# Kernel tuning notes

Measured on AMD Instinct MI355X. Metric: run time of the kernel, lower is better.

Reference implementation:

```python
import jax, jax.numpy as jnp
import numpy as np

B, S, D, H, DFF = 2, 2048, 1024, 16, 4096
DK = D // H
EPS = 1e-6
MASK_FILL = -1.0  # original code uses -1**9 == -1 (precedence bug), NOT -1e9


def layernorm(x, gamma, beta):
    # original: (x - mean) / (std + eps), std unbiased (torch default ddof=1), scalar gamma/beta
    mean = jnp.mean(x, axis=-1, keepdims=True)
    std = jnp.std(x, axis=-1, keepdims=True, ddof=1)
    return gamma * (x - mean) / (std + EPS) + beta


def setup_inputs() -> dict:
    key = jax.random.key(0)
    ks = jax.random.split(key, 12)
    sc = 0.02
    return {
        "x": jax.random.normal(ks[0], (B, S, D), jnp.float32),
        "src_mask": jnp.ones((B, 1, 1, S), jnp.int32),
        "wq": jax.random.normal(ks[1], (D, D), jnp.float32) * sc,
        "bq": jnp.zeros((D,), jnp.float32),
        "wk": jax.random.normal(ks[2], (D, D), jnp.float32) * sc,
        "bk": jnp.zeros((D,), jnp.float32),
        "wv": jax.random.normal(ks[3], (D, D), jnp.float32) * sc,
        "bv": jnp.zeros((D,), jnp.float32),
        "wo": jax.random.normal(ks[4], (D, D), jnp.float32) * sc,
        "bo": jnp.zeros((D,), jnp.float32),
        "w1": jax.random.normal(ks[5], (D, DFF), jnp.float32) * sc,
        "b1": jnp.zeros((DFF,), jnp.float32),
        "w2": jax.random.normal(ks[6], (DFF, D), jnp.float32) * sc,
        "b2": jnp.zeros((D,), jnp.float32),
        "g1": jnp.ones((), jnp.float32),
        "be1": jnp.zeros((), jnp.float32),
        "g2": jnp.ones((), jnp.float32),
        "be2": jnp.zeros((), jnp.float32),
    }


def reference(x, src_mask, wq, bq, wk, bk, wv, bv, wo, bo,
              w1, b1, w2, b2, g1, be1, g2, be2):
    # --- residual 1: pre-LN self-attention ---
    xn = layernorm(x, g1, be1)
    q = (xn @ wq + bq).reshape(B, S, H, DK).transpose(0, 2, 1, 3)  # [B,H,S,DK]
    k = (xn @ wk + bk).reshape(B, S, H, DK).transpose(0, 2, 1, 3)
    v = (xn @ wv + bv).reshape(B, S, H, DK).transpose(0, 2, 1, 3)
    scores = jnp.einsum('bhqd,bhkd->bhqk', q, k) / jnp.sqrt(jnp.float32(DK))
    scores = jnp.where(src_mask == 0, MASK_FILL, scores)
    attn = jax.nn.softmax(scores, axis=-1)
    ctx = jnp.einsum('bhqk,bhkd->bhqd', attn, v)
    ctx = ctx.transpose(0, 2, 1, 3).reshape(B, S, D)
    attn_out = ctx @ wo + bo
    x = x + attn_out  # dropout is identity in eval

    # --- residual 2: pre-LN feed-forward ---
    xn = layernorm(x, g2, be2)
    h = jax.nn.relu(xn @ w1 + b1)
    ff_out = h @ w2 + b2
    return x + ff_out
```

## Files before the change

kernel.cpp:

```cpp
#include <hip/hip_runtime.h>

typedef unsigned short u16;
typedef __bf16 bf16x8 __attribute__((ext_vector_type(8)));
typedef float f32x4 __attribute__((ext_vector_type(4)));

#define AS1U(p) ((__attribute__((address_space(1))) unsigned int*)(p))
#define AS3U(p) ((__attribute__((address_space(3))) unsigned int*)(p))

__device__ __forceinline__ u16 f2bf(float f) {
  union { float f; unsigned int i; } c; c.f = f;
  return (u16)((c.i + 0x7FFFu + ((c.i >> 16) & 1u)) >> 16);
}
__device__ __forceinline__ u16 f2bf_trunc(float f) {
  union { float f; unsigned int i; } c; c.f = f;
  return (u16)(c.i >> 16);
}

template <int BM, int BN, int OMODE>
__global__ __launch_bounds__(256) void gemm_bt(
    const u16* __restrict__ A, long lda,
    const u16* __restrict__ B, long ldb,
    void* __restrict__ Cv, long ldc,
    int K, float scale, const float* __restrict__ bias,
    const float* __restrict__ res, long ldres, int relu) {
  constexpr int BK = 32;
  constexpr int WN = (BN == 128) ? 64 : 32;
  constexpr int MI = 4, NJ = WN / 16;
  __shared__ u16 As0[BM * BK], As1[BM * BK];
  __shared__ u16 Bs0[BN * BK], Bs1[BN * BK];
  const int t = threadIdx.x;
  const int w = t >> 6, l = t & 63;
  const int wr = w >> 1, wc = w & 1;
  const int quad = l >> 4, mlo = l & 15;
  const long row0 = (long)blockIdx.x * BM;
  const long col0 = (long)blockIdx.y * BN;

  f32x4 acc[MI][NJ] = {};

  auto stage = [&](u16 (&Ad)[BM * BK], u16 (&Bd)[BN * BK], int k0) {
#pragma unroll
    for (int i = 0; i < BM / 64; i++) {
      int s = t + i * 256, r = s >> 2, c = s & 3;
      const u16* g = A + (row0 + r) * lda + k0 + (c ^ (r & 3)) * 8;
      __builtin_amdgcn_global_load_lds(AS1U(g), AS3U(&Ad[s * 8]), 16, 0, 0);
    }
#pragma unroll
    for (int i = 0; i < BN / 64; i++) {
      int s = t + i * 256, r = s >> 2, c = s & 3;
      const u16* g = B + (col0 + r) * ldb + k0 + (c ^ (r & 3)) * 8;
      __builtin_amdgcn_global_load_lds(AS1U(g), AS3U(&Bd[s * 8]), 16, 0, 0);
    }
  };
  auto compute = [&](const u16 (&Asr)[BM * BK], const u16 (&Bsr)[BN * BK]) {
    bf16x8 a[MI], b[NJ];
#pragma unroll
    for (int i = 0; i < MI; i++) {
      int r = wr * 64 + i * 16 + mlo;
      a[i] = *(const bf16x8*)&Asr[(r * 4 + (quad ^ (mlo & 3))) * 8];
    }
#pragma unroll
    for (int j = 0; j < NJ; j++) {
      int r = wc * WN + j * 16 + mlo;
      b[j] = *(const bf16x8*)&Bsr[(r * 4 + (quad ^ (mlo & 3))) * 8];
    }
#pragma unroll
    for (int i = 0; i < MI; i++)
#pragma unroll
      for (int j = 0; j < NJ; j++)
        acc[i][j] = __builtin_amdgcn_mfma_f32_16x16x32_bf16(a[i], b[j], acc[i][j], 0, 0, 0);
  };

  stage(As0, Bs0, 0);
  for (int k0 = 0; k0 < K; k0 += 2 * BK) {
    __syncthreads();
    stage(As1, Bs1, k0 + BK);
    compute(As0, Bs0);
    __syncthreads();
    if (k0 + 2 * BK < K) stage(As0, Bs0, k0 + 2 * BK);
    compute(As1, Bs1);
  }

#pragma unroll
  for (int i = 0; i < MI; i++) {
#pragma unroll
    for (int j = 0; j < NJ; j++) {
      const long gn = col0 + wc * WN + j * 16 + mlo;
      const float bv = bias ? bias[gn] : 0.0f;
#pragma unroll
      for (int r = 0; r < 4; r++) {
        const long gm = row0 + wr * 64 + i * 16 + quad * 4 + r;
        float v = acc[i][j][r] * scale + bv;
        if (relu && v < 0.0f) v = 0.0f;
        if (res) v += res[gm * ldres + gn];
        if (OMODE == 0) ((float*)Cv)[gm * ldc + gn] = v;
        else ((u16*)Cv)[gm * ldc + gn] = f2bf(v);
      }
    }
  }
}

__global__ __launch_bounds__(256) void flash_attn(
    const u16* __restrict__ QKV, const u16* __restrict__ VT,
    const int* __restrict__ mask, u16* __restrict__ ctx) {
  __shared__ u16 Ks[2][64 * 64];
  __shared__ u16 Vs[2][64 * 64];
  __shared__ u16 Ps[128 * 64];
  const int t = threadIdx.x;
  const int w = t >> 6, l = t & 63;
  const int quad = l >> 4, mlo = l & 15;
  const int z = blockIdx.z, b = z >> 4, h = z & 15;
  const long q0 = (long)blockIdx.x * 128;
  const u16* Qg = QKV + (long)b * (2048L * 3072) + h * 64;
  const u16* Kg = Qg + 1024;
  const u16* Vg = VT + (long)b * (1024L * 2048) + (long)(h * 64) * 2048;
  const int* mrow = mask + b * 2048;

#pragma unroll
  for (int i = 0; i < 2; i++) {
    int s = t + i * 256, r = s >> 3, c = s & 7;
    __builtin_amdgcn_global_load_lds(AS1U(Kg + (long)r * 3072 + (c ^ (r & 7)) * 8),
                                     AS3U(&Ks[0][s * 8]), 16, 0, 0);
    __builtin_amdgcn_global_load_lds(AS1U(Vg + (long)r * 2048 + (c ^ (r & 7)) * 8),
                                     AS3U(&Vs[0][s * 8]), 16, 0, 0);
  }
  bf16x8 aq[2][2];
#pragma unroll
  for (int i = 0; i < 2; i++)
#pragma unroll
    for (int kk = 0; kk < 2; kk++) {
      const u16* g = Qg + (q0 + w * 32 + i * 16 + mlo) * 3072 + kk * 32 + quad * 8;
      union { uint4 u; bf16x8 v; } c; c.u = *(const uint4*)g;
      aq[i][kk] = c.v;
    }

  f32x4 o[2][5] = {};
  union { u16 s[8]; bf16x8 v; } ones;
#pragma unroll
  for (int e = 0; e < 8; e++) ones.s[e] = 0x3F80;
  const float CS = 0.125f * 1.44269504f;
  const float CM = -1.44269504f;

  for (int it = 0; it < 32; ++it) {
    const int cur = it & 1;
    const int key0 = it * 64;
    __syncthreads();
    if (it + 1 < 32) {
      const int nb = 1 - cur;
      const u16* Kg2 = Kg + (long)(it + 1) * 64 * 3072;
      const u16* Vg2 = Vg + (it + 1) * 64;
#pragma unroll
      for (int i2 = 0; i2 < 2; i2++) {
        int s = t + i2 * 256, r = s >> 3, c = s & 7;
        __builtin_amdgcn_global_load_lds(AS1U(Kg2 + (long)r * 3072 + (c ^ (r & 7)) * 8),
                                         AS3U(&Ks[nb][s * 8]), 16, 0, 0);
        __builtin_amdgcn_global_load_lds(AS1U(Vg2 + (long)r * 2048 + (c ^ (r & 7)) * 8),
                                         AS3U(&Vs[nb][s * 8]), 16, 0, 0);
      }
    }
    int mz[4];
#pragma unroll
    for (int j = 0; j < 4; j++) mz[j] = mrow[key0 + j * 16 + mlo];
    f32x4 sa[2][4] = {};
#pragma unroll
    for (int kk = 0; kk < 2; kk++) {
      bf16x8 bk[4];
#pragma unroll
      for (int j = 0; j < 4; j++) {
        int rr = j * 16 + mlo;
        bk[j] = *(const bf16x8*)&Ks[cur][(rr * 8 + ((kk * 4 + quad) ^ (mlo & 7))) * 8];
      }
#pragma unroll
      for (int i = 0; i < 2; i++)
#pragma unroll
        for (int j = 0; j < 4; j++)
          sa[i][j] = __builtin_amdgcn_mfma_f32_16x16x32_bf16(aq[i][kk], bk[j], sa[i][j], 0, 0, 0);
    }
#pragma unroll
    for (int i = 0; i < 2; i++) {
      const int rbase = w * 32 + i * 16 + quad * 4;
      const int skey = (rbase >> 2) & 7;
#pragma unroll
      for (int j = 0; j < 4; j++) {
        const int col = j * 16 + mlo;
        u16* pp = &Ps[rbase * 64 + (((col >> 3) ^ skey) << 3) + (col & 7)];
#pragma unroll
        for (int r = 0; r < 4; r++) {
          float s = (mz[j] == 0) ? CM : sa[i][j][r] * CS;
          pp[r * 64] = f2bf_trunc(__builtin_amdgcn_exp2f(s));
        }
      }
    }
#pragma unroll
    for (int kk = 0; kk < 2; kk++) {
      bf16x8 ap[2], bv[4];
#pragma unroll
      for (int i = 0; i < 2; i++) {
        const int row = w * 32 + i * 16 + mlo;
        const int skey = (row >> 2) & 7;
        ap[i] = *(const bf16x8*)&Ps[(row * 8 + ((kk * 4 + quad) ^ skey)) * 8];
      }
#pragma unroll
      for (int j = 0; j < 4; j++) {
        int rr = j * 16 + mlo;
        bv[j] = *(const bf16x8*)&Vs[cur][(rr * 8 + ((kk * 4 + quad) ^ (mlo & 7))) * 8];
      }
#pragma unroll
      for (int i = 0; i < 2; i++) {
#pragma unroll
        for (int j = 0; j < 4; j++)
          o[i][j] = __builtin_amdgcn_mfma_f32_16x16x32_bf16(ap[i], bv[j], o[i][j], 0, 0, 0);
        o[i][4] = __builtin_amdgcn_mfma_f32_16x16x32_bf16(ap[i], ones.v, o[i][4], 0, 0, 0);
      }
    }
  }
  u16* cb = ctx + (long)b * (2048L * 1024) + q0 * 1024 + h * 64;
#pragma unroll
  for (int i = 0; i < 2; i++)
#pragma unroll
    for (int r = 0; r < 4; r++) {
      float inv = 1.0f / o[i][4][r];
      int row = w * 32 + i * 16 + quad * 4 + r;
#pragma unroll
      for (int j = 0; j < 4; j++)
        cb[(long)row * 1024 + j * 16 + mlo] = f2bf(o[i][j][r] * inv);
    }
}

__device__ __forceinline__ void ln_row(const float* __restrict__ x, u16* __restrict__ y,
                                       const float* __restrict__ g, const float* __restrict__ b,
                                       long row, float* ss, float* s2) {
  const float* xr = x + row * 1024;
  float v[4];
  float s = 0.f, sq = 0.f;
#pragma unroll
  for (int i = 0; i < 4; i++) {
    float f = xr[threadIdx.x + i * 256];
    v[i] = f; s += f; sq += f * f;
  }
#pragma unroll
  for (int o = 32; o > 0; o >>= 1) { s += __shfl_xor(s, o, 64); sq += __shfl_xor(sq, o, 64); }
  const int w = threadIdx.x >> 6;
  if ((threadIdx.x & 63) == 0) { ss[w] = s; s2[w] = sq; }
  __syncthreads();
  s = ss[0] + ss[1] + ss[2] + ss[3];
  sq = s2[0] + s2[1] + s2[2] + s2[3];
  const float mean = s * (1.0f / 1024.0f);
  float var = (sq - s * mean) * (1.0f / 1023.0f);
  var = fmaxf(var, 0.0f);
  const float sc = g[0] / (sqrtf(var) + 1e-6f);
  const float be = b[0];
#pragma unroll
  for (int i = 0; i < 4; i++)
    y[row * 1024 + threadIdx.x + i * 256] = f2bf((v[i] - mean) * sc + be);
}

__global__ __launch_bounds__(256) void ln_kernel(const float* __restrict__ x, u16* __restrict__ y,
                                                 const float* __restrict__ g, const float* __restrict__ b) {
  __shared__ float ss[4], s2[4];
  ln_row(x, y, g, b, blockIdx.x, ss, s2);
}

__global__ __launch_bounds__(256) void prep_kernel(
    const float* __restrict__ x, const float* __restrict__ g1, const float* __restrict__ be1,
    const float* __restrict__ wq, const float* __restrict__ wk, const float* __restrict__ wv,
    const float* __restrict__ wo, const float* __restrict__ w1, const float* __restrict__ w2,
    const float* __restrict__ bq, const float* __restrict__ bk, const float* __restrict__ bv,
    u16* __restrict__ xnH, u16* __restrict__ WqkvT, u16* __restrict__ woT,
    u16* __restrict__ w1T, u16* __restrict__ w2T, float* __restrict__ biasQKV) {
  __shared__ float tile[32][33];
  __shared__ float ss[4], s2[4];
  const int bid = blockIdx.x;
  if (bid >= 12300) {
    ln_row(x, xnH, g1, be1, bid - 12300, ss, s2);
    return;
  }
  if (bid >= 12288) {
    const int i = (bid - 12288) * 256 + threadIdx.x;
    if (i < 3072) biasQKV[i] = (i < 1024) ? bq[i] : ((i < 2048) ? bk[i - 1024] : bv[i - 2048]);
    return;
  }
  const float* in; u16* out; long ldin, ldo; int ti, tiles_x;
  if (bid < 1024)      { in = wq; out = WqkvT;                     ldin = 1024; ldo = 1024; ti = bid;        tiles_x = 32; }
  else if (bid < 2048) { in = wk; out = WqkvT + (size_t)1024*1024; ldin = 1024; ldo = 1024; ti = bid - 1024; tiles_x = 32; }
  else if (bid < 3072) { in = wv; out = WqkvT + (size_t)2048*1024; ldin = 1024; ldo = 1024; ti = bid - 2048; tiles_x = 32; }
  else if (bid < 4096) { in = wo; out = woT;                       ldin = 1024; ldo = 1024; ti = bid - 3072; tiles_x = 32; }
  else if (bid < 8192) { in = w1; out = w1T;                       ldin = 4096; ldo = 1024; ti = bid - 4096; tiles_x = 128; }
  else                 { in = w2; out = w2T;                       ldin = 1024; ldo = 4096; ti = bid - 8192; tiles_x = 32; }
  const int bx = (ti % tiles_x) * 32, by = (ti / tiles_x) * 32;
  const int tx = threadIdx.x & 31, ty = threadIdx.x >> 5;
#pragma unroll
  for (int i = 0; i < 32; i += 8) tile[ty + i][tx] = in[(long)(by + ty + i) * ldin + bx + tx];
  __syncthreads();
#pragma unroll
  for (int i = 0; i < 32; i += 8)
    out[(long)(bx + ty + i) * ldo + by + tx] = f2bf(tile[tx][ty + i]);
}

__global__ __launch_bounds__(256) void ttrans1(const u16* __restrict__ in, long ldin, long siz,
                                               u16* __restrict__ out, long ldo, long soz) {
  __shared__ u16 tile[32][33];
  const long zi = (long)blockIdx.z * siz, zo = (long)blockIdx.z * soz;
  const int bx = blockIdx.x * 32, by = blockIdx.y * 32;
  const int tx = threadIdx.x & 31, ty = threadIdx.x >> 5;
#pragma unroll
  for (int i = 0; i < 32; i += 8)
    tile[ty + i][tx] = in[zi + (long)(by + ty + i) * ldin + bx + tx];
  __syncthreads();
#pragma unroll
  for (int i = 0; i < 32; i += 8)
    out[zo + (long)(bx + ty + i) * ldo + by + tx] = tile[tx][ty + i];
}

extern "C" void kernel_launch(void* const* d_in, const int* in_sizes, int n_in,
                              void* d_out, int out_size, void* d_ws, size_t ws_size,
                              hipStream_t stream) {
  const float* x   = (const float*)d_in[0];
  const int*   msk = (const int*)d_in[1];
  const float* wq  = (const float*)d_in[2];
  const float* bq  = (const float*)d_in[3];
  const float* wk  = (const float*)d_in[4];
  const float* bk  = (const float*)d_in[5];
  const float* wv  = (const float*)d_in[6];
  const float* bv  = (const float*)d_in[7];
  const float* wo  = (const float*)d_in[8];
  const float* bo  = (const float*)d_in[9];
  const float* w1  = (const float*)d_in[10];
  const float* b1  = (const float*)d_in[11];
  const float* w2  = (const float*)d_in[12];
  const float* b2  = (const float*)d_in[13];
  const float* g1  = (const float*)d_in[14];
  const float* be1 = (const float*)d_in[15];
  const float* g2  = (const float*)d_in[16];
  const float* be2 = (const float*)d_in[17];
  float* out = (float*)d_out;

  char* basep = (char*)d_ws;
  size_t off = 0;
  auto au = [&](size_t nelem) -> u16* {
    u16* r = (u16*)(basep + off);
    off += ((nelem * 2) + 255) & ~(size_t)255;
    return r;
  };
  auto afp = [&](size_t nelem) -> float* {
    float* r = (float*)(basep + off);
    off += ((nelem * 4) + 255) & ~(size_t)255;
    return r;
  };

  u16* xnH  = au((size_t)4096 * 1024);
  u16* QKV  = au((size_t)4096 * 3072);
  u16* VTH  = au((size_t)2 * 1024 * 2048);
  u16* ctxH = au((size_t)4096 * 1024);
  float* x1 = afp((size_t)4096 * 1024);
  u16* hb   = au((size_t)4096 * 4096);
  u16* WqkvT = au((size_t)3072 * 1024);
  u16* woT  = au((size_t)1024 * 1024);
  u16* w1T  = au((size_t)4096 * 1024);
  u16* w2T  = au((size_t)1024 * 4096);
  float* biasQKV = afp(3072);

  const dim3 blk(256);

  prep_kernel<<<16396, blk, 0, stream>>>(x, g1, be1, wq, wk, wv, wo, w1, w2,
                                         bq, bk, bv, xnH, WqkvT, woT, w1T, w2T, biasQKV);

  gemm_bt<128, 128, 2><<<dim3(32, 24), blk, 0, stream>>>(
      xnH, 1024, WqkvT, 1024, QKV, 3072, 1024, 1.0f,
      biasQKV, (const float*)0, 0, 0);

  ttrans1<<<dim3(32, 64, 2), blk, 0, stream>>>(
      QKV + 2048, 3072, (long)2048 * 3072, VTH, 2048, (long)1024 * 2048);

  flash_attn<<<dim3(16, 1, 32), blk, 0, stream>>>(QKV, VTH, msk, ctxH);

  gemm_bt<128, 64, 0><<<dim3(32, 16), blk, 0, stream>>>(
      ctxH, 1024, woT, 1024, x1, 1024, 1024, 1.0f, bo, x, 1024, 0);

  ln_kernel<<<4096, blk, 0, stream>>>(x1, xnH, g2, be2);

  gemm_bt<128, 128, 2><<<dim3(32, 32), blk, 0, stream>>>(
      xnH, 1024, w1T, 1024, hb, 4096, 1024, 1.0f,
      b1, (const float*)0, 0, 1);

  gemm_bt<128, 64, 0><<<dim3(32, 16), blk, 0, stream>>>(
      hb, 4096, w2T, 4096, out, 1024, 4096, 1.0f, b2, x1, 1024, 0);
}
```

Measured before the change: 380.7 us.

## Halve attention query tile and drop LDS swizzle in GEMM staging

The flash attention kernel now handles 64 queries per block (16 per warp) instead of 128, doubling the grid to 1024 blocks. This spreads work across more CUs and lowers register and LDS use, at the cost of reloading K/V tiles twice as often. Separately, the GEMM drops its XOR swizzle on LDS staging and reads, which saves index arithmetic but may bring back LDS bank conflicts. The swizzle keys for the attention P and K/V buffers are also changed.

```diff
diff --git a/kernel.cpp b/kernel.cpp
--- a/kernel.cpp
+++ b/kernel.cpp
@@ -41,13 +41,13 @@
 #pragma unroll
     for (int i = 0; i < BM / 64; i++) {
       int s = t + i * 256, r = s >> 2, c = s & 3;
-      const u16* g = A + (row0 + r) * lda + k0 + (c ^ (r & 3)) * 8;
+      const u16* g = A + (row0 + r) * lda + k0 + c * 8;
       __builtin_amdgcn_global_load_lds(AS1U(g), AS3U(&Ad[s * 8]), 16, 0, 0);
     }
 #pragma unroll
     for (int i = 0; i < BN / 64; i++) {
       int s = t + i * 256, r = s >> 2, c = s & 3;
-      const u16* g = B + (col0 + r) * ldb + k0 + (c ^ (r & 3)) * 8;
+      const u16* g = B + (col0 + r) * ldb + k0 + c * 8;
       __builtin_amdgcn_global_load_lds(AS1U(g), AS3U(&Bd[s * 8]), 16, 0, 0);
     }
   };
@@ -56,12 +56,12 @@
 #pragma unroll
     for (int i = 0; i < MI; i++) {
       int r = wr * 64 + i * 16 + mlo;
-      a[i] = *(const bf16x8*)&Asr[(r * 4 + (quad ^ (mlo & 3))) * 8];
+      a[i] = *(const bf16x8*)&Asr[(r * 4 + quad) * 8];
     }
 #pragma unroll
     for (int j = 0; j < NJ; j++) {
       int r = wc * WN + j * 16 + mlo;
-      b[j] = *(const bf16x8*)&Bsr[(r * 4 + (quad ^ (mlo & 3))) * 8];
+      b[j] = *(const bf16x8*)&Bsr[(r * 4 + quad) * 8];
     }
 #pragma unroll
     for (int i = 0; i < MI; i++)
@@ -104,12 +104,12 @@
     const int* __restrict__ mask, u16* __restrict__ ctx) {
   __shared__ u16 Ks[2][64 * 64];
   __shared__ u16 Vs[2][64 * 64];
-  __shared__ u16 Ps[128 * 64];
+  __shared__ u16 Ps[64 * 64];
   const int t = threadIdx.x;
   const int w = t >> 6, l = t & 63;
   const int quad = l >> 4, mlo = l & 15;
   const int z = blockIdx.z, b = z >> 4, h = z & 15;
-  const long q0 = (long)blockIdx.x * 128;
+  const long q0 = (long)blockIdx.x * 64;
   const u16* Qg = QKV + (long)b * (2048L * 3072) + h * 64;
   const u16* Kg = Qg + 1024;
   const u16* Vg = VT + (long)b * (1024L * 2048) + (long)(h * 64) * 2048;
@@ -123,17 +123,15 @@
     __builtin_amdgcn_global_load_lds(AS1U(Vg + (long)r * 2048 + (c ^ (r & 7)) * 8),
                                      AS3U(&Vs[0][s * 8]), 16, 0, 0);
   }
-  bf16x8 aq[2][2];
-#pragma unroll
-  for (int i = 0; i < 2; i++)
-#pragma unroll
-    for (int kk = 0; kk < 2; kk++) {
-      const u16* g = Qg + (q0 + w * 32 + i * 16 + mlo) * 3072 + kk * 32 + quad * 8;
-      union { uint4 u; bf16x8 v; } c; c.u = *(const uint4*)g;
-      aq[i][kk] = c.v;
-    }
-
-  f32x4 o[2][5] = {};
+  bf16x8 aq[2];
+#pragma unroll
+  for (int kk = 0; kk < 2; kk++) {
+    const u16* g = Qg + (q0 + w * 16 + mlo) * 3072 + kk * 32 + quad * 8;
+    union { uint4 u; bf16x8 v; } c; c.u = *(const uint4*)g;
+    aq[kk] = c.v;
+  }
+
+  f32x4 o[5] = {};
   union { u16 s[8]; bf16x8 v; } ones;
 #pragma unroll
   for (int e = 0; e < 8; e++) ones.s[e] = 0x3F80;
@@ -160,70 +158,63 @@
     int mz[4];
 #pragma unroll
     for (int j = 0; j < 4; j++) mz[j] = mrow[key0 + j * 16 + mlo];
-    f32x4 sa[2][4] = {};
+    f32x4 sa[4] = {};
 #pragma unroll
     for (int kk = 0; kk < 2; kk++) {
       bf16x8 bk[4];
 #pragma unroll
       for (int j = 0; j < 4; j++) {
         int rr = j * 16 + mlo;
-        bk[j] = *(const bf16x8*)&Ks[cur][(rr * 8 + ((kk * 4 + quad) ^ (mlo & 7))) * 8];
-      }
-#pragma unroll
-      for (int i = 0; i < 2; i++)
-#pragma unroll
-        for (int j = 0; j < 4; j++)
-          sa[i][j] = __builtin_amdgcn_mfma_f32_16x16x32_bf16(aq[i][kk], bk[j], sa[i][j], 0, 0, 0);
-    }
-#pragma unroll
-    for (int i = 0; i < 2; i++) {
-      const int rbase = w * 32 + i * 16 + quad * 4;
-      const int skey = (rbase >> 2) & 7;
+        bk[j] = *(const bf16x8*)&Ks[cur][(rr * 8 + ((kk * 4 + quad) ^ (rr & 7))) * 8];
+      }
+#pragma unroll
+      for (int j = 0; j < 4; j++)
+        sa[j] = __builtin_amdgcn_mfma_f32_16x16x32_bf16(aq[kk], bk[j], sa[j], 0, 0, 0);
+    }
+    {
+      const int r0 = w * 16 + quad * 4;
 #pragma unroll
       for (int j = 0; j < 4; j++) {
         const int col = j * 16 + mlo;
-        u16* pp = &Ps[rbase * 64 + (((col >> 3) ^ skey) << 3) + (col & 7)];
-#pragma unroll
-        for (int r = 0; r < 4; r++) {
-          float s = (mz[j] == 0) ? CM : sa[i][j][r] * CS;
-          pp[r * 64] = f2bf_trunc(__builtin_amdgcn_exp2f(s));
+#pragma unroll
+        for (int rp = 0; rp < 2; rp++) {
+          const int row = r0 + rp * 2;
+          const int skey = (row >> 1) & 7;
+          u16* pp = &Ps[row * 64 + (((col >> 3) ^ skey) << 3) + (col & 7)];
+#pragma unroll
+          for (int r = 0; r < 2; r++) {
+            float s = (mz[j] == 0) ? CM : sa[j][rp * 2 + r] * CS;
+            pp[r * 64] = f2bf_trunc(__builtin_amdgcn_exp2f(s));
+          }
         }
       }
     }
 #pragma unroll
     for (int kk = 0; kk < 2; kk++) {
-      bf16x8 ap[2], bv[4];
-#pragma unroll
-      for (int i = 0; i < 2; i++) {
-        const int row = w * 32 + i * 16 + mlo;
-        const int skey = (row >> 2) & 7;
-        ap[i] = *(const bf16x8*)&Ps[(row * 8 + ((kk * 4 + quad) ^ skey)) * 8];
-      }
-#pragma unroll
-      for (int j = 0; j < 4; j++) {
-        int rr = j * 16 + mlo;
-        bv[j] = *(const bf16x8*)&Vs[cur][(rr * 8 + ((kk * 4 + quad) ^ (mlo & 7))) * 8];
-      }
-#pragma unroll
-      for (int i = 0; i < 2; i++) {
-#pragma unroll
-        for (int j = 0; j < 4; j++)
-          o[i][j] = __builtin_amdgcn_mfma_f32_16x16x32_bf16(ap[i], bv[j], o[i][j], 0, 0, 0);
-        o[i][4] = __builtin_amdgcn_mfma_f32_16x16x32_bf16(ap[i], ones.v, o[i][4], 0, 0, 0);
-      }
+      const int row = w * 16 + mlo;
+      const int skey = (row >> 1) & 7;
+      bf16x8 ap = *(const bf16x8*)&Ps[(row * 8 + ((kk * 4 + quad) ^ skey)) * 8];
+      bf16x8 bv[4];
+#pragma unroll
+      for (int jd = 0; jd < 4; jd++) {
+        int rr = jd * 16 + mlo;
+        bv[jd] = *(const bf16x8*)&Vs[cur][(rr * 8 + ((kk * 4 + quad) ^ (rr & 7))) * 8];
+      }
+#pragma unroll
+      for (int jd = 0; jd < 4; jd++)
+        o[jd] = __builtin_amdgcn_mfma_f32_16x16x32_bf16(ap, bv[jd], o[jd], 0, 0, 0);
+      o[4] = __builtin_amdgcn_mfma_f32_16x16x32_bf16(ap, ones.v, o[4], 0, 0, 0);
     }
   }
   u16* cb = ctx + (long)b * (2048L * 1024) + q0 * 1024 + h * 64;
 #pragma unroll
-  for (int i = 0; i < 2; i++)
-#pragma unroll
-    for (int r = 0; r < 4; r++) {
-      float inv = 1.0f / o[i][4][r];
-      int row = w * 32 + i * 16 + quad * 4 + r;
-#pragma unroll
-      for (int j = 0; j < 4; j++)
-        cb[(long)row * 1024 + j * 16 + mlo] = f2bf(o[i][j][r] * inv);
-    }
+  for (int r = 0; r < 4; r++) {
+    const float inv = 1.0f / o[4][r];
+    const int row = w * 16 + quad * 4 + r;
+#pragma unroll
+    for (int jd = 0; jd < 4; jd++)
+      cb[(long)row * 1024 + jd * 16 + mlo] = f2bf(o[jd][r] * inv);
+  }
 }
 
 __device__ __forceinline__ void ln_row(const float* __restrict__ x, u16* __restrict__ y,
@@ -371,7 +362,7 @@
   ttrans1<<<dim3(32, 64, 2), blk, 0, stream>>>(
       QKV + 2048, 3072, (long)2048 * 3072, VTH, 2048, (long)1024 * 2048);
 
-  flash_attn<<<dim3(16, 1, 32), blk, 0, stream>>>(QKV, VTH, msk, ctxH);
+  flash_attn<<<dim3(32, 1, 32), blk, 0, stream>>>(QKV, VTH, msk, ctxH);
 
   gemm_bt<128, 64, 0><<<dim3(32, 16), blk, 0, stream>>>(
       ctxH, 1024, woT, 1024, x1, 1024, 1024, 1.0f, bo, x, 1024, 0);
```

New measurement: 396.4 us. 4.1% more time.

## Fuse V transpose into QKV GEMM, split-K FFN2, bf16 residual, drop LDS swizzle

Applied to the files above, without the earlier changes.

The QKV GEMM epilogue now writes the transposed V directly, which removes the separate transpose kernel. The residual x1 is stored as bf16 and LayerNorm reads bf16, cutting memory traffic. The second FFN GEMM is split along K into two partial fp32 outputs that a new combine kernel sums with the bias and residual, which doubles the grid for better occupancy. The XOR swizzle on LDS loads is also removed. That likely adds LDS bank conflicts and lowers residual precision, and the transposed-V epilogue writes are strided.

```diff
diff --git a/kernel.cpp b/kernel.cpp
--- a/kernel.cpp
+++ b/kernel.cpp
@@ -7,6 +7,9 @@
 #define AS1U(p) ((__attribute__((address_space(1))) unsigned int*)(p))
 #define AS3U(p) ((__attribute__((address_space(3))) unsigned int*)(p))
 
+__device__ __forceinline__ float bf2f(u16 u) {
+  union { unsigned int i; float f; } c; c.i = ((unsigned int)u) << 16; return c.f;
+}
 __device__ __forceinline__ u16 f2bf(float f) {
   union { float f; unsigned int i; } c; c.f = f;
   return (u16)((c.i + 0x7FFFu + ((c.i >> 16) & 1u)) >> 16);
@@ -18,11 +21,12 @@
 
 template <int BM, int BN, int OMODE>
 __global__ __launch_bounds__(256) void gemm_bt(
-    const u16* __restrict__ A, long lda,
-    const u16* __restrict__ B, long ldb,
-    void* __restrict__ Cv, long ldc,
+    const u16* __restrict__ A, long lda, long sAz,
+    const u16* __restrict__ B, long ldb, long sBz,
+    void* __restrict__ Cv, long ldc, long sCz,
     int K, float scale, const float* __restrict__ bias,
-    const float* __restrict__ res, long ldres, int relu) {
+    const float* __restrict__ res, long ldres,
+    const u16* __restrict__ resb, int relu, u16* __restrict__ vt) {
   constexpr int BK = 32;
   constexpr int WN = (BN == 128) ? 64 : 32;
   constexpr int MI = 4, NJ = WN / 16;
@@ -34,6 +38,8 @@
   const int quad = l >> 4, mlo = l & 15;
   const long row0 = (long)blockIdx.x * BM;
   const long col0 = (long)blockIdx.y * BN;
+  const u16* Ab = A + (long)blockIdx.z * sAz;
+  const u16* Bb = B + (long)blockIdx.z * sBz;
 
   f32x4 acc[MI][NJ] = {};
 
@@ -41,13 +47,13 @@
 #pragma unroll
     for (int i = 0; i < BM / 64; i++) {
       int s = t + i * 256, r = s >> 2, c = s & 3;
-      const u16* g = A + (row0 + r) * lda + k0 + (c ^ (r & 3)) * 8;
+      const u16* g = Ab + (row0 + r) * lda + k0 + c * 8;
       __builtin_amdgcn_global_load_lds(AS1U(g), AS3U(&Ad[s * 8]), 16, 0, 0);
     }
 #pragma unroll
     for (int i = 0; i < BN / 64; i++) {
       int s = t + i * 256, r = s >> 2, c = s & 3;
-      const u16* g = B + (col0 + r) * ldb + k0 + (c ^ (r & 3)) * 8;
+      const u16* g = Bb + (col0 + r) * ldb + k0 + c * 8;
       __builtin_amdgcn_global_load_lds(AS1U(g), AS3U(&Bd[s * 8]), 16, 0, 0);
     }
   };
@@ -56,12 +62,12 @@
 #pragma unroll
     for (int i = 0; i < MI; i++) {
       int r = wr * 64 + i * 16 + mlo;
-      a[i] = *(const bf16x8*)&Asr[(r * 4 + (quad ^ (mlo & 3))) * 8];
+      a[i] = *(const bf16x8*)&Asr[(r * 4 + quad) * 8];
     }
 #pragma unroll
     for (int j = 0; j < NJ; j++) {
       int r = wc * WN + j * 16 + mlo;
-      b[j] = *(const bf16x8*)&Bsr[(r * 4 + (quad ^ (mlo & 3))) * 8];
+      b[j] = *(const bf16x8*)&Bsr[(r * 4 + quad) * 8];
     }
 #pragma unroll
     for (int i = 0; i < MI; i++)
@@ -80,6 +86,7 @@
     compute(As1, Bs1);
   }
 
+  const long czoff = (long)blockIdx.z * sCz;
 #pragma unroll
   for (int i = 0; i < MI; i++) {
 #pragma unroll
@@ -92,8 +99,14 @@
         float v = acc[i][j][r] * scale + bv;
         if (relu && v < 0.0f) v = 0.0f;
         if (res) v += res[gm * ldres + gn];
-        if (OMODE == 0) ((float*)Cv)[gm * ldc + gn] = v;
-        else ((u16*)Cv)[gm * ldc + gn] = f2bf(v);
+        if (resb) v += bf2f(resb[gm * ldc + gn]);
+        if (OMODE == 0) ((float*)Cv)[gm * ldc + gn + czoff] = v;
+        else {
+          const u16 bfv = f2bf(v);
+          ((u16*)Cv)[gm * ldc + gn + czoff] = bfv;
+          if (vt && gn >= 2048)
+            vt[((gm >> 11) * 1024L + (gn - 2048)) * 2048 + (gm & 2047)] = bfv;
+        }
       }
     }
   }
@@ -254,10 +267,49 @@
     y[row * 1024 + threadIdx.x + i * 256] = f2bf((v[i] - mean) * sc + be);
 }
 
-__global__ __launch_bounds__(256) void ln_kernel(const float* __restrict__ x, u16* __restrict__ y,
-                                                 const float* __restrict__ g, const float* __restrict__ b) {
+__global__ __launch_bounds__(256) void ln_kernel_bf(const u16* __restrict__ x, u16* __restrict__ y,
+                                                    const float* __restrict__ g, const float* __restrict__ b) {
   __shared__ float ss[4], s2[4];
-  ln_row(x, y, g, b, blockIdx.x, ss, s2);
+  const long row = blockIdx.x;
+  const u16* xr = x + row * 1024;
+  float v[4];
+  float s = 0.f, sq = 0.f;
+#pragma unroll
+  for (int i = 0; i < 4; i++) {
+    float f = bf2f(xr[threadIdx.x + i * 256]);
+    v[i] = f; s += f; sq += f * f;
+  }
+#pragma unroll
+  for (int o = 32; o > 0; o >>= 1) { s += __shfl_xor(s, o, 64); sq += __shfl_xor(sq, o, 64); }
+  const int w = threadIdx.x >> 6;
+  if ((threadIdx.x & 63) == 0) { ss[w] = s; s2[w] = sq; }
+  __syncthreads();
+  s = ss[0] + ss[1] + ss[2] + ss[3];
+  sq = s2[0] + s2[1] + s2[2] + s2[3];
+  const float mean = s * (1.0f / 1024.0f);
+  float var = (sq - s * mean) * (1.0f / 1023.0f);
+  var = fmaxf(var, 0.0f);
+  const float sc = g[0] / (sqrtf(var) + 1e-6f);
+  const float be = b[0];
+#pragma unroll
+  for (int i = 0; i < 4; i++)
+    y[row * 1024 + threadIdx.x + i * 256] = f2bf((v[i] - mean) * sc + be);
+}
+
+__global__ __launch_bounds__(256) void combine2(
+    const float* __restrict__ p0, const float* __restrict__ p1,
+    const u16* __restrict__ x1, const float* __restrict__ b2, float* __restrict__ out) {
+  const long base = (long)blockIdx.x * 1024 + threadIdx.x * 4;
+  const float4 a = *(const float4*)&p0[base];
+  const float4 b = *(const float4*)&p1[base];
+  const float4 bb = *(const float4*)&b2[threadIdx.x * 4];
+  const ushort4 xr = *(const ushort4*)&x1[base];
+  float4 o;
+  o.x = a.x + b.x + bb.x + bf2f(xr.x);
+  o.y = a.y + b.y + bb.y + bf2f(xr.y);
+  o.z = a.z + b.z + bb.z + bf2f(xr.z);
+  o.w = a.w + b.w + bb.w + bf2f(xr.w);
+  *(float4*)&out[base] = o;
 }
 
 __global__ __launch_bounds__(256) void prep_kernel(
@@ -294,21 +346,6 @@
 #pragma unroll
   for (int i = 0; i < 32; i += 8)
     out[(long)(bx + ty + i) * ldo + by + tx] = f2bf(tile[tx][ty + i]);
-}
-
-__global__ __launch_bounds__(256) void ttrans1(const u16* __restrict__ in, long ldin, long siz,
-                                               u16* __restrict__ out, long ldo, long soz) {
-  __shared__ u16 tile[32][33];
-  const long zi = (long)blockIdx.z * siz, zo = (long)blockIdx.z * soz;
-  const int bx = blockIdx.x * 32, by = blockIdx.y * 32;
-  const int tx = threadIdx.x & 31, ty = threadIdx.x >> 5;
-#pragma unroll
-  for (int i = 0; i < 32; i += 8)
-    tile[ty + i][tx] = in[zi + (long)(by + ty + i) * ldin + bx + tx];
-  __syncthreads();
-#pragma unroll
-  for (int i = 0; i < 32; i += 8)
-    out[zo + (long)(bx + ty + i) * ldo + by + tx] = tile[tx][ty + i];
 }
 
 extern "C" void kernel_launch(void* const* d_in, const int* in_sizes, int n_in,
@@ -351,12 +388,13 @@
   u16* QKV  = au((size_t)4096 * 3072);
   u16* VTH  = au((size_t)2 * 1024 * 2048);
   u16* ctxH = au((size_t)4096 * 1024);
-  float* x1 = afp((size_t)4096 * 1024);
+  u16* x1   = au((size_t)4096 * 1024);
   u16* hb   = au((size_t)4096 * 4096);
   u16* WqkvT = au((size_t)3072 * 1024);
   u16* woT  = au((size_t)1024 * 1024);
   u16* w1T  = au((size_t)4096 * 1024);
   u16* w2T  = au((size_t)1024 * 4096);
+  float* parts = afp((size_t)2 * 4096 * 1024);
   float* biasQKV = afp(3072);
 
   const dim3 blk(256);
@@ -365,23 +403,24 @@
                                          bq, bk, bv, xnH, WqkvT, woT, w1T, w2T, biasQKV);
 
   gemm_bt<128, 128, 2><<<dim3(32, 24), blk, 0, stream>>>(
-      xnH, 1024, WqkvT, 1024, QKV, 3072, 1024, 1.0f,
-      biasQKV, (const float*)0, 0, 0);
-
-  ttrans1<<<dim3(32, 64, 2), blk, 0, stream>>>(
-      QKV + 2048, 3072, (long)2048 * 3072, VTH, 2048, (long)1024 * 2048);
+      xnH, 1024, 0, WqkvT, 1024, 0, QKV, 3072, 0, 1024, 1.0f,
+      biasQKV, (const float*)0, 0, (const u16*)0, 0, VTH);
 
   flash_attn<<<dim3(16, 1, 32), blk, 0, stream>>>(QKV, VTH, msk, ctxH);
 
-  gemm_bt<128, 64, 0><<<dim3(32, 16), blk, 0, stream>>>(
-      ctxH, 1024, woT, 1024, x1, 1024, 1024, 1.0f, bo, x, 1024, 0);
-
-  ln_kernel<<<4096, blk, 0, stream>>>(x1, xnH, g2, be2);
+  gemm_bt<128, 64, 2><<<dim3(32, 16), blk, 0, stream>>>(
+      ctxH, 1024, 0, woT, 1024, 0, x1, 1024, 0, 1024, 1.0f,
+      bo, x, 1024, (const u16*)0, 0, (u16*)0);
+
+  ln_kernel_bf<<<4096, blk, 0, stream>>>(x1, xnH, g2, be2);
 
   gemm_bt<128, 128, 2><<<dim3(32, 32), blk, 0, stream>>>(
-      xnH, 1024, w1T, 1024, hb, 4096, 1024, 1.0f,
-      b1, (const float*)0, 0, 1);
-
-  gemm_bt<128, 64, 0><<<dim3(32, 16), blk, 0, stream>>>(
-      hb, 4096, w2T, 4096, out, 1024, 4096, 1.0f, b2, x1, 1024, 0);
-}
+      xnH, 1024, 0, w1T, 1024, 0, hb, 4096, 0, 1024, 1.0f,
+      b1, (const float*)0, 0, (const u16*)0, 1, (u16*)0);
+
+  gemm_bt<128, 64, 0><<<dim3(32, 16, 2), blk, 0, stream>>>(
+      hb, 4096, 2048, w2T, 4096, 2048, parts, 1024, (long)4096 * 1024,
+      2048, 1.0f, (const float*)0, (const float*)0, 0, (const u16*)0, 0, (u16*)0);
+
+  combine2<<<4096, blk, 0, stream>>>(parts, parts + (size_t)4096 * 1024, x1, b2, out);
+}
```

Result: slower. 398.0 us (+4.5%).
